# Performance work log

Hardware: AMD Instinct MI355X
Metric: run time of the kernel (lower is better)

## Reference

```python
import jax, jax.numpy as jnp
import numpy as np
import math

D = 128  # embedding_dim, hard-coded in source


def setup_inputs() -> dict:
    key = jax.random.key(0)
    k1, k2, k3, k4, k5 = jax.random.split(key, 5)
    B, S = 4, 4096
    x = jax.random.normal(k1, (B, S, D), dtype=jnp.float32)
    token_attention_masks = jax.random.randint(k2, (B, S), 0, 2).astype(jnp.int64)
    # torch.rand -> uniform [0,1)
    w_query = jax.random.uniform(k3, (D, D), dtype=jnp.float32)
    w_key = jax.random.uniform(k4, (D, D), dtype=jnp.float32)
    w_value = jax.random.uniform(k5, (D, D), dtype=jnp.float32)
    return {
        "x": x,
        "token_attention_masks": token_attention_masks,
        "w_query": w_query,
        "w_key": w_key,
        "w_value": w_value,
    }


def reference(x, token_attention_masks, w_query, w_key, w_value):
    # QKV projections (single head, no bias)
    query = jnp.einsum('bsd,de->bse', x, w_query)
    key = jnp.einsum('bsd,de,->bse', x, w_key, jnp.float32(1.0)) if False else jnp.einsum('bsd,de->bse', x, w_key)
    value = jnp.einsum('bsd,de->bse', x, w_value)
    dk = key.shape[2]
    scale = jnp.einsum('bqd,bkd->bqk', query, key) / math.sqrt(dk)  # [B,S,S]
    # NOTE: the original module computes an additive mask (`new_scale`) but
    # applies softmax to the UNMASKED `scale` (a bug in the source); we
    # replicate the actual output math faithfully, so the mask is unused.
    attention_probability = jax.nn.softmax(scale, axis=2)
    attention_output = jnp.einsum('bqk,bkd->bqd', attention_probability, value)
    return attention_output
```

## Files before the change

### kernel.cpp

```cpp
#include <hip/hip_runtime.h>
#include <math.h>

#define BATCH  4
#define SEQ    4096
#define DIM    128
#define NROW   (BATCH*SEQ)
#define NSPLIT 4

typedef _Float16 f16_t;
typedef _Float16 f16x2  __attribute__((ext_vector_type(2)));
typedef _Float16 f16x4  __attribute__((ext_vector_type(4)));
typedef _Float16 f16x8  __attribute__((ext_vector_type(8)));
typedef _Float16 f16x16 __attribute__((ext_vector_type(16)));
typedef float    f32x4  __attribute__((ext_vector_type(4)));
typedef float    f32x16 __attribute__((ext_vector_type(16)));

#define QSCALE ((float)(1.4426950408889634 / 11.313708498984761))

#define LDXX 72
#define LDW  68
#define LDE 136

__global__ __launch_bounds__(256, 3) void proj_kernel(
    const float* __restrict__ x,
    const float* __restrict__ wq, const float* __restrict__ wk,
    const float* __restrict__ wv,
    f16_t* __restrict__ Qh, f16_t* __restrict__ Kh, f16_t* __restrict__ Vt)
{
    __shared__ __align__(16) f16_t smem[(64+64)*LDXX + (128+128)*LDW];
    f16_t* sXh = smem;
    f16_t* sXl = smem + 64*LDXX;
    f16_t* sWh = smem + 128*LDXX;
    f16_t* sWl = smem + 128*LDXX + 128*LDW;

    const int tid  = threadIdx.x;
    const int wave = tid >> 6;
    const int lane = tid & 63;
    const int quad = lane >> 4;
    const int ln   = lane & 15;

    const int nt = blockIdx.x % 3;
    const int mb = blockIdx.x / 3;
    const int m0 = mb * 64;
    const float* __restrict__ w = (nt == 0) ? wq : ((nt == 1) ? wk : wv);

    const int k0j[2] = { ((tid      ) >> 5) * 4, ((tid + 256) >> 5) * 4 };
    const int n4j[2] = { (tid       ) & 31,      (tid + 256) & 31       };

    f32x4 acc[8];
    #pragma unroll
    for (int nb = 0; nb < 8; nb++)
        for (int r = 0; r < 4; r++) acc[nb][r] = 0.f;

    float4 px[4];
    float  pw[2][16];
    auto load_phase = [&](int ph) {
        #pragma unroll
        for (int i = 0; i < 4; i++) {
            const int idx = tid + 256*i;
            px[i] = *(const float4*)(x + (size_t)(m0+(idx>>4))*DIM + ph*64 + (idx&15)*4);
        }
        #pragma unroll
        for (int j = 0; j < 2; j++)
            #pragma unroll
            for (int e = 0; e < 4; e++)
                *(float4*)&pw[j][e*4] =
                    *(const float4*)(w + (size_t)(ph*64 + k0j[j] + e)*DIM + n4j[j]*4);
    };
    load_phase(0);

    #pragma unroll
    for (int ph = 0; ph < 2; ph++) {
        __syncthreads();
        #pragma unroll
        for (int i = 0; i < 4; i++) {
            const int idx = tid + 256*i;
            const int r = idx >> 4, f4 = idx & 15;
            const float4 v = px[i];
            f16_t h0=(f16_t)v.x, h1=(f16_t)v.y, h2=(f16_t)v.z, h3=(f16_t)v.w;
            *(f16x4*)(sXh + r*LDXX + f4*4) = (f16x4){h0,h1,h2,h3};
            *(f16x4*)(sXl + r*LDXX + f4*4) =
                (f16x4){(f16_t)(v.x-(float)h0),(f16_t)(v.y-(float)h1),
                        (f16_t)(v.z-(float)h2),(f16_t)(v.w-(float)h3)};
        }
        #pragma unroll
        for (int j = 0; j < 2; j++) {
            #pragma unroll
            for (int c = 0; c < 4; c++) {
                const int n = n4j[j]*4 + c;
                f16x4 hp, lp;
                #pragma unroll
                for (int e = 0; e < 4; e++) {
                    const float v = pw[j][e*4 + c];
                    const f16_t hh = (f16_t)v;
                    hp[e] = hh;
                    lp[e] = (f16_t)(v - (float)hh);
                }
                *(f16x4*)(sWh + n*LDW + k0j[j]) = hp;
                *(f16x4*)(sWl + n*LDW + k0j[j]) = lp;
            }
        }
        if (ph == 0) load_phase(1);
        __syncthreads();

        f16x8 ah[2], al[2];
        #pragma unroll
        for (int ks = 0; ks < 2; ks++) {
            ah[ks] = *(const f16x8*)(sXh + (wave*16+ln)*LDXX + quad*8 + ks*32);
            al[ks] = *(const f16x8*)(sXl + (wave*16+ln)*LDXX + quad*8 + ks*32);
        }
        #pragma unroll
        for (int nb = 0; nb < 8; nb++) {
            #pragma unroll
            for (int ks = 0; ks < 2; ks++) {
                const f16_t* wb = sWh + (nb*16+ln)*LDW + quad*8 + ks*32;
                const f16x4 b0 = *(const f16x4*)(wb);
                const f16x4 b1 = *(const f16x4*)(wb + 4);
                const f16x8 bh = __builtin_shufflevector(b0, b1, 0,1,2,3,4,5,6,7);
                const f16_t* wc = sWl + (nb*16+ln)*LDW + quad*8 + ks*32;
                const f16x4 c0 = *(const f16x4*)(wc);
                const f16x4 c1 = *(const f16x4*)(wc + 4);
                const f16x8 bl = __builtin_shufflevector(c0, c1, 0,1,2,3,4,5,6,7);
                acc[nb] = __builtin_amdgcn_mfma_f32_16x16x32_f16(ah[ks], bh, acc[nb], 0,0,0);
                acc[nb] = __builtin_amdgcn_mfma_f32_16x16x32_f16(al[ks], bh, acc[nb], 0,0,0);
                acc[nb] = __builtin_amdgcn_mfma_f32_16x16x32_f16(ah[ks], bl, acc[nb], 0,0,0);
            }
        }
    }

    __syncthreads();

    if (nt != 2) {
        const float scale = (nt == 0) ? QSCALE : 1.0f;
        f16_t* dsth = (nt == 0) ? Qh : Kh;
        f16_t* sH = smem;
        #pragma unroll
        for (int nb = 0; nb < 8; nb++)
            #pragma unroll
            for (int r = 0; r < 4; r++) {
                const int row  = wave*16 + quad*4 + r;
                const int colp = (nb*16 + ln) ^ (quad << 4);
                sH[row*LDE + colp] = (f16_t)(acc[nb][r] * scale);
            }
        __syncthreads();
        #pragma unroll
        for (int jj = 0; jj < 4; jj++) {
            const int c    = tid + 256*jj;
            const int row  = c >> 4;
            const int col  = (c & 15) * 8;
            const int colp = col ^ (((row >> 2) & 3) << 4);
            *(uint4*)(dsth + (size_t)(m0 + row)*DIM + col) =
                *(const uint4*)(sH + row*LDE + colp);
        }
    } else {
        f16_t* svt = smem;
        const int rowl = wave*16 + quad*4;
        #pragma unroll
        for (int nb = 0; nb < 8; nb++)
            for (int r = 0; r < 4; r++)
                svt[(nb*16+ln)*LDXX + rowl + r] = (f16_t)acc[nb][r];
        __syncthreads();
        const int bb = m0 >> 12, sloc = m0 & (SEQ-1);
        const int d = tid >> 1, half = tid & 1;
        #pragma unroll
        for (int q = 0; q < 4; q++) {
            *(uint4*)(Vt + ((size_t)bb*DIM + d)*SEQ + sloc + half*32 + q*8) =
                *(const uint4*)(svt + d*LDXX + half*32 + q*8);
        }
    }
}

#define LDK 136
#define LDV 68
#define LDO 132

__global__ __launch_bounds__(256, 3) void flash_kernel(
    const f16_t* __restrict__ Qh, const f16_t* __restrict__ Kh,
    const f16_t* __restrict__ Vt,
    f16_t* __restrict__ Opart, float2* __restrict__ mlbuf)
{
    __shared__ __align__(16) f16_t smem[64*LDK + 128*LDV];
    f16_t* sK = smem;
    f16_t* sV = smem + 64*LDK;

    const int tid  = threadIdx.x;
    const int wave = tid >> 6;
    const int lane = tid & 63;
    const int l31  = lane & 31;
    const int h    = lane >> 5;

    const int grp = blockIdx.x & 15;
    const int b   = grp >> 2;
    const int sp  = grp & 3;
    const int qt  = blockIdx.x >> 4;
    const int q0  = qt*128 + wave*32;

    f16x8 qf[8];
    {
        const f16_t* gq = Qh + ((size_t)b*SEQ + q0 + l31)*DIM + h*8;
        #pragma unroll
        for (int ks = 0; ks < 8; ks++)
            qf[ks] = *(const f16x8*)(gq + ks*16);
    }

    f32x16 oacc[4];
    #pragma unroll
    for (int mb = 0; mb < 4; mb++)
        #pragma unroll
        for (int r = 0; r < 16; r++) oacc[mb][r] = 0.f;
    float mrun = -__builtin_inff(), lrun = 0.f;

    const int kr = tid >> 4;
    const int kc = (tid & 15) * 8;
    const int vd = tid >> 3;
    const int vj = (tid & 7) * 8;

    const f16_t* gK = Kh + (size_t)b*SEQ*DIM;
    const f16_t* gV = Vt + (size_t)b*DIM*SEQ;

    for (int kt = sp*16; kt < sp*16 + 16; kt++) {
        float4 pk[4], pv[4];
        {
            const f16_t* gk = gK + (size_t)kt*64*DIM;
            const f16_t* gv = gV + kt*64;
            #pragma unroll
            for (int p = 0; p < 4; p++)
                pk[p] = *(const float4*)(gk + (kr + 16*p)*DIM + kc);
            #pragma unroll
            for (int p = 0; p < 4; p++)
                pv[p] = *(const float4*)(gv + (size_t)(vd + 32*p)*SEQ + vj);
        }
        __syncthreads();
        #pragma unroll
        for (int p = 0; p < 4; p++)
            *(uint4*)(sK + (kr+16*p)*LDK + kc) = __builtin_bit_cast(uint4, pk[p]);
        #pragma unroll
        for (int p = 0; p < 4; p++) {
            const f16x8 w = __builtin_bit_cast(f16x8, pv[p]);
            *(f16x4*)(sV + (vd+32*p)*LDV + vj    ) = __builtin_shufflevector(w, w, 0,1,2,3);
            *(f16x4*)(sV + (vd+32*p)*LDV + vj + 4) = __builtin_shufflevector(w, w, 4,5,6,7);
        }
        __syncthreads();

        f32x16 sacc[2];
        #pragma unroll
        for (int sb = 0; sb < 2; sb++)
            #pragma unroll
            for (int r = 0; r < 16; r++) sacc[sb][r] = 0.f;
        #pragma unroll
        for (int ks = 0; ks < 8; ks++) {
            #pragma unroll
            for (int sb = 0; sb < 2; sb++) {
                const f16x8 af = *(const f16x8*)(sK + (sb*32 + l31)*LDK + ks*16 + h*8);
                sacc[sb] = __builtin_amdgcn_mfma_f32_32x32x16_f16(af, qf[ks], sacc[sb], 0,0,0);
            }
        }

        float mx = sacc[0][0];
        #pragma unroll
        for (int sb = 0; sb < 2; sb++)
            #pragma unroll
            for (int r = 0; r < 16; r++) mx = fmaxf(mx, sacc[sb][r]);
        mx = fmaxf(mx, __shfl_xor(mx, 32, 64));
        const float mnew = fmaxf(mrun, mx);

        if (__any(mnew > mrun)) {
            const float alpha = __builtin_amdgcn_exp2f(mrun - mnew);
            lrun *= alpha;
            #pragma unroll
            for (int mb = 0; mb < 4; mb++)
                #pragma unroll
                for (int r = 0; r < 16; r++) oacc[mb][r] *= alpha;
            mrun = mnew;
        }

        if (__all(mx < mrun - 25.f)) continue;

        union PBuf { f16x2 p2[8]; f16x8 v8[2]; } pbf[2];
        float rs = 0.f;
        #pragma unroll
        for (int sb = 0; sb < 2; sb++)
            #pragma unroll
            for (int r2 = 0; r2 < 8; r2++) {
                const float e0 = __builtin_amdgcn_exp2f(sacc[sb][2*r2]   - mnew);
                const float e1 = __builtin_amdgcn_exp2f(sacc[sb][2*r2+1] - mnew);
                rs += e0 + e1;
                pbf[sb].p2[r2] = __builtin_bit_cast(f16x2,
                    __builtin_amdgcn_cvt_pkrtz(e0, e1));
            }
        rs += __shfl_xor(rs, 32, 64);
        lrun += rs;

        #pragma unroll
        for (int t = 0; t < 4; t++) {
            const f16x8 pb = pbf[t>>1].v8[t&1];
            #pragma unroll
            for (int mb = 0; mb < 4; mb++) {
                const f16_t* va = sV + (mb*32 + l31)*LDV + t*16 + h*4;
                const f16x4 a0 = *(const f16x4*)(va);
                const f16x4 a1 = *(const f16x4*)(va + 8);
                const f16x8 af = __builtin_shufflevector(a0, a1, 0,1,2,3,4,5,6,7);
                oacc[mb] = __builtin_amdgcn_mfma_f32_32x32x16_f16(af, pb, oacc[mb], 0,0,0);
            }
        }
    }

    __syncthreads();
    const float invl = 1.f / lrun;
    f16_t* sOw = smem + wave*32*LDO;
    #pragma unroll
    for (int mb = 0; mb < 4; mb++)
        #pragma unroll
        for (int rp = 0; rp < 8; rp++) {
            const int r0 = rp*2;
            const int d  = mb*32 + (r0 & 3) + 8*(r0 >> 2) + 4*h;
            union { f16_t f[2]; unsigned u; } pkv;
            pkv.f[0] = (f16_t)(oacc[mb][r0]   * invl);
            pkv.f[1] = (f16_t)(oacc[mb][r0+1] * invl);
            *(unsigned*)(sOw + l31*LDO + d) = pkv.u;
        }
    __asm__ volatile("s_waitcnt lgkmcnt(0)" ::: "memory");

    const size_t gb = ((size_t)sp*NROW + (size_t)b*SEQ + q0)*DIM;
    #pragma unroll
    for (int jj = 0; jj < 8; jj++) {
        const int c  = lane + 64*jj;
        const int q  = c >> 4;
        const int dc = (c & 15)*8;
        union { f16x4 v[2]; uint4 u; } o;
        o.v[0] = *(const f16x4*)(sOw + q*LDO + dc);
        o.v[1] = *(const f16x4*)(sOw + q*LDO + dc + 4);
        *(uint4*)(Opart + gb + (size_t)q*DIM + dc) = o.u;
    }
    if (h == 0)
        mlbuf[sp*NROW + b*SEQ + q0 + l31] = make_float2(mrun, lrun);
}

__global__ __launch_bounds__(256) void combine_kernel(
    const f16_t* __restrict__ Opart, const float2* __restrict__ mlbuf,
    float* __restrict__ out)
{
    const int idx = blockIdx.x*256 + threadIdx.x;
    const int row = idx >> 4;
    const int d0  = (idx & 15) * 8;

    float m[NSPLIT], l[NSPLIT];
    #pragma unroll
    for (int s = 0; s < NSPLIT; s++) {
        const float2 v = mlbuf[s*NROW + row];
        m[s] = v.x; l[s] = v.y;
    }
    float M = m[0];
    #pragma unroll
    for (int s = 1; s < NSPLIT; s++) M = fmaxf(M, m[s]);
    float w[NSPLIT], denom = 0.f;
    #pragma unroll
    for (int s = 0; s < NSPLIT; s++) {
        w[s] = l[s] * __builtin_amdgcn_exp2f(m[s] - M);
        denom += w[s];
    }
    const float inv = 1.f / denom;

    float o[8] = {0,0,0,0,0,0,0,0};
    #pragma unroll
    for (int s = 0; s < NSPLIT; s++) {
        const f16x8 v = *(const f16x8*)(Opart + ((size_t)s*NROW + row)*DIM + d0);
        const float ws = w[s] * inv;
        #pragma unroll
        for (int j = 0; j < 8; j++) o[j] += ws * (float)v[j];
    }
    float* ob = out + (size_t)row*DIM + d0;
    *(float4*)(ob)     = make_float4(o[0], o[1], o[2], o[3]);
    *(float4*)(ob + 4) = make_float4(o[4], o[5], o[6], o[7]);
}

extern "C" void kernel_launch(void* const* d_in, const int* in_sizes, int n_in,
                              void* d_out, int out_size, void* d_ws, size_t ws_size,
                              hipStream_t stream) {
    const float* x  = (const float*)d_in[0];
    const float* wq = (const float*)d_in[2];
    const float* wk = (const float*)d_in[3];
    const float* wv = (const float*)d_in[4];

    f16_t* ws = (f16_t*)d_ws;
    f16_t* Qh    = ws;
    f16_t* Kh    = Qh  + (size_t)NROW*DIM;
    f16_t* Vt    = Kh  + (size_t)NROW*DIM;
    f16_t* Opart = Vt  + (size_t)NROW*DIM;
    float2* mlbuf = (float2*)(Opart + (size_t)NSPLIT*NROW*DIM);

    proj_kernel   <<<(NROW/64)*3,           256, 0, stream>>>(x, wq, wk, wv, Qh, Kh, Vt);
    flash_kernel  <<<BATCH*(SEQ/128)*NSPLIT,256, 0, stream>>>(Qh, Kh, Vt, Opart, mlbuf);
    combine_kernel<<<NROW*DIM/8/256,        256, 0, stream>>>(Opart, mlbuf, (float*)d_out);
}
```

Before: 121.2 us.

## Double-buffer K/V tiles in LDS to overlap global loads with MFMA compute

Splits shared memory into two halves and prefetches the next K/V tile into registers while the current tile's QK and PV MFMAs run, then stores it to the alternate LDS buffer. This drops to a single barrier per iteration and is meant to hide global load latency. LDS use doubles to about 69 KB per block, which may lower how many blocks fit per CU at the launch bound of 3. The prefetch registers also stay live across the compute and add register pressure.

```diff
diff --git a/kernel.cpp b/kernel.cpp
--- a/kernel.cpp
+++ b/kernel.cpp
@@ -173,16 +173,14 @@
 #define LDK 136
 #define LDV 68
 #define LDO 132
+#define HALF (64*LDK + 128*LDV)
 
 __global__ __launch_bounds__(256, 3) void flash_kernel(
     const f16_t* __restrict__ Qh, const f16_t* __restrict__ Kh,
     const f16_t* __restrict__ Vt,
     f16_t* __restrict__ Opart, float2* __restrict__ mlbuf)
 {
-    __shared__ __align__(16) f16_t smem[64*LDK + 128*LDV];
-    f16_t* sK = smem;
-    f16_t* sV = smem + 64*LDK;
-
+    __shared__ __align__(16) f16_t smem[2*HALF];
     const int tid  = threadIdx.x;
     const int wave = tid >> 6;
     const int lane = tid & 63;
@@ -218,29 +216,48 @@
     const f16_t* gK = Kh + (size_t)b*SEQ*DIM;
     const f16_t* gV = Vt + (size_t)b*DIM*SEQ;
 
-    for (int kt = sp*16; kt < sp*16 + 16; kt++) {
-        float4 pk[4], pv[4];
-        {
-            const f16_t* gk = gK + (size_t)kt*64*DIM;
-            const f16_t* gv = gV + kt*64;
-            #pragma unroll
-            for (int p = 0; p < 4; p++)
-                pk[p] = *(const float4*)(gk + (kr + 16*p)*DIM + kc);
-            #pragma unroll
-            for (int p = 0; p < 4; p++)
-                pv[p] = *(const float4*)(gv + (size_t)(vd + 32*p)*SEQ + vj);
-        }
-        __syncthreads();
+    const int kt0 = sp*16, kend = sp*16 + 16;
+
+    float4 pk[4], pv[4];
+    auto load_k = [&](int kt) {
+        const f16_t* gk = gK + (size_t)kt*64*DIM;
+        #pragma unroll
+        for (int p = 0; p < 4; p++)
+            pk[p] = *(const float4*)(gk + (kr + 16*p)*DIM + kc);
+    };
+    auto load_v = [&](int kt) {
+        const f16_t* gv = gV + kt*64;
+        #pragma unroll
+        for (int p = 0; p < 4; p++)
+            pv[p] = *(const float4*)(gv + (size_t)(vd + 32*p)*SEQ + vj);
+    };
+    auto store_k = [&](f16_t* sK) {
         #pragma unroll
         for (int p = 0; p < 4; p++)
             *(uint4*)(sK + (kr+16*p)*LDK + kc) = __builtin_bit_cast(uint4, pk[p]);
+    };
+    auto store_v = [&](f16_t* sV) {
         #pragma unroll
         for (int p = 0; p < 4; p++) {
             const f16x8 w = __builtin_bit_cast(f16x8, pv[p]);
             *(f16x4*)(sV + (vd+32*p)*LDV + vj    ) = __builtin_shufflevector(w, w, 0,1,2,3);
             *(f16x4*)(sV + (vd+32*p)*LDV + vj + 4) = __builtin_shufflevector(w, w, 4,5,6,7);
         }
-        __syncthreads();
+    };
+
+    load_k(kt0); load_v(kt0);
+    store_k(smem); store_v(smem + 64*LDK);
+    __syncthreads();
+
+    for (int kt = kt0; kt < kend; kt++) {
+        const int cur = (kt - kt0) & 1;
+        f16_t* sKc = smem + cur*HALF;
+        f16_t* sVc = sKc + 64*LDK;
+        f16_t* sKn = smem + (cur^1)*HALF;
+        f16_t* sVn = sKn + 64*LDK;
+        const bool more = (kt + 1 < kend);
+
+        if (more) load_k(kt + 1);
 
         f32x16 sacc[2];
         #pragma unroll
@@ -251,10 +268,11 @@
         for (int ks = 0; ks < 8; ks++) {
             #pragma unroll
             for (int sb = 0; sb < 2; sb++) {
-                const f16x8 af = *(const f16x8*)(sK + (sb*32 + l31)*LDK + ks*16 + h*8);
+                const f16x8 af = *(const f16x8*)(sKc + (sb*32 + l31)*LDK + ks*16 + h*8);
                 sacc[sb] = __builtin_amdgcn_mfma_f32_32x32x16_f16(af, qf[ks], sacc[sb], 0,0,0);
             }
         }
+        if (more) { store_k(sKn); load_v(kt + 1); }
 
         float mx = sacc[0][0];
         #pragma unroll
@@ -274,38 +292,41 @@
             mrun = mnew;
         }
 
-        if (__all(mx < mrun - 25.f)) continue;
-
-        union PBuf { f16x2 p2[8]; f16x8 v8[2]; } pbf[2];
-        float rs = 0.f;
-        #pragma unroll
-        for (int sb = 0; sb < 2; sb++)
-            #pragma unroll
-            for (int r2 = 0; r2 < 8; r2++) {
-                const float e0 = __builtin_amdgcn_exp2f(sacc[sb][2*r2]   - mnew);
-                const float e1 = __builtin_amdgcn_exp2f(sacc[sb][2*r2+1] - mnew);
-                rs += e0 + e1;
-                pbf[sb].p2[r2] = __builtin_bit_cast(f16x2,
-                    __builtin_amdgcn_cvt_pkrtz(e0, e1));
+        if (more) store_v(sVn);
+
+        if (!__all(mx < mrun - 25.f)) {
+            union PBuf { f16x2 p2[8]; f16x8 v8[2]; } pbf[2];
+            float rs = 0.f;
+            #pragma unroll
+            for (int sb = 0; sb < 2; sb++)
+                #pragma unroll
+                for (int r2 = 0; r2 < 8; r2++) {
+                    const float e0 = __builtin_amdgcn_exp2f(sacc[sb][2*r2]   - mnew);
+                    const float e1 = __builtin_amdgcn_exp2f(sacc[sb][2*r2+1] - mnew);
+                    rs += e0 + e1;
+                    pbf[sb].p2[r2] = __builtin_bit_cast(f16x2,
+                        __builtin_amdgcn_cvt_pkrtz(e0, e1));
+                }
+            rs += __shfl_xor(rs, 32, 64);
+            lrun += rs;
+
+            #pragma unroll
+            for (int t = 0; t < 4; t++) {
+                const f16x8 pb = pbf[t>>1].v8[t&1];
+                #pragma unroll
+                for (int mb = 0; mb < 4; mb++) {
+                    const f16_t* va = sVc + (mb*32 + l31)*LDV + t*16 + h*4;
+                    const f16x4 a0 = *(const f16x4*)(va);
+                    const f16x4 a1 = *(const f16x4*)(va + 8);
+                    const f16x8 af = __builtin_shufflevector(a0, a1, 0,1,2,3,4,5,6,7);
+                    oacc[mb] = __builtin_amdgcn_mfma_f32_32x32x16_f16(af, pb, oacc[mb], 0,0,0);
+                }
             }
-        rs += __shfl_xor(rs, 32, 64);
-        lrun += rs;
-
-        #pragma unroll
-        for (int t = 0; t < 4; t++) {
-            const f16x8 pb = pbf[t>>1].v8[t&1];
-            #pragma unroll
-            for (int mb = 0; mb < 4; mb++) {
-                const f16_t* va = sV + (mb*32 + l31)*LDV + t*16 + h*4;
-                const f16x4 a0 = *(const f16x4*)(va);
-                const f16x4 a1 = *(const f16x4*)(va + 8);
-                const f16x8 af = __builtin_shufflevector(a0, a1, 0,1,2,3,4,5,6,7);
-                oacc[mb] = __builtin_amdgcn_mfma_f32_32x32x16_f16(af, pb, oacc[mb], 0,0,0);
-            }
-        }
-    }
-
-    __syncthreads();
+        }
+
+        __syncthreads();
+    }
+
     const float invl = 1.f / lrun;
     f16_t* sOw = smem + wave*32*LDO;
     #pragma unroll
```

Result: slower. 143.7 us (+18.5%).
